# Kernel optimization log

Hardware: AMD Instinct MI355X
Metric: run time of the kernel (lower is better)

## Reference

```python
import jax, jax.numpy as jnp
import numpy as np

N = 50000
E = 800000
D = 64
H = 128


def setup_inputs() -> dict:
    key = jax.random.key(0)
    ks = jax.random.split(key, 8)
    x1 = jax.random.normal(ks[0], (N, D), dtype=jnp.float32)
    x2 = jax.random.normal(ks[1], (N, D), dtype=jnp.float32)
    edge_index1 = jax.random.randint(ks[2], (2, E), 0, N, dtype=jnp.int32)
    edge_index2 = jax.random.randint(ks[3], (2, E), 0, N, dtype=jnp.int32)
    W1 = jax.random.normal(ks[4], (2 * D, H), dtype=jnp.float32) * (1.0 / np.sqrt(2 * D))
    b1 = jnp.zeros((H,), dtype=jnp.float32)
    W2 = jax.random.normal(ks[5], (H, D), dtype=jnp.float32) * (1.0 / np.sqrt(H))
    b2 = jnp.zeros((D,), dtype=jnp.float32)
    return {"x1": x1, "x2": x2, "edge_index1": edge_index1, "edge_index2": edge_index2,
            "W1": W1, "b1": b1, "W2": W2, "b2": b2}


def _mlp(e, W1, b1, W2, b2):
    # edge MLP: Linear -> ReLU -> Linear
    h = jax.nn.relu(e @ W1 + b1)
    return h @ W2 + b2


def _scatter_max(vals, row, dim_size):
    # scatter-max aggregation; empty segments (which pyg scatter_ fills with 0)
    out = jax.ops.segment_max(vals, row, num_segments=dim_size)
    return jnp.where(jnp.isfinite(out), out, 0.0)


def reference(x1, x2, edge_index1, edge_index2, W1, b1, W2, b2):
    row1, col1 = edge_index1[0], edge_index1[1]
    # edge features from x1 -> x1: [E, 2D]
    e1 = jnp.concatenate([x1[row1], x1[col1] - x1[row1]], axis=1)
    out1 = _scatter_max(_mlp(e1, W1, b1, W2, b2), row1, x1.shape[0])

    row2, col2 = edge_index2[0], edge_index2[1]
    # edge features from x1 -> x2: [E, 2D]
    e2 = jnp.concatenate([x1[row2], x2[col2] - x1[row2]], axis=1)
    out2 = _scatter_max(_mlp(e2, W1, b1, W2, b2), row2, x2.shape[0])

    return jnp.concatenate([out1, out2], axis=-1)  # [N, 2*D]
```

## Files before the change

### kernel.cpp

```cpp
#include <hip/hip_runtime.h>

#define NN 50000
#define EE 800000
#define NTILES 12500
#define BPG 512
#define NPB 196

typedef _Float16 half8 __attribute__((ext_vector_type(8)));
typedef __attribute__((ext_vector_type(4))) float f32x4;
typedef __attribute__((ext_vector_type(4))) unsigned u32x4;

__device__ __forceinline__ unsigned enc(float f) {
    unsigned u = __float_as_uint(f);
    return u ^ (unsigned)(((int)u >> 31) | 0x80000000);
}
__device__ __forceinline__ float dec(unsigned u) {
    unsigned v = (u & 0x80000000u) ? (u & 0x7FFFFFFFu) : ~u;
    return __uint_as_float(v);
}

__global__ void decode_acc(unsigned* __restrict__ acc, int n) {
    int i = blockIdx.x * blockDim.x + threadIdx.x;
    if (i < n) {
        unsigned u = acc[i];
        ((float*)acc)[i] = (u == 0u) ? 0.0f : dec(u);
    }
}

__global__ __launch_bounds__(256)
void pre_k(const float* __restrict__ x1, const float* __restrict__ x2,
           const float* __restrict__ W1, const float* __restrict__ b1,
           _Float16* __restrict__ pre)
{
    const int j  = blockIdx.x / NPB;
    const int bb = blockIdx.x % NPB;
    const float* __restrict__ xs = (j == 2) ? x2 : x1;
    _Float16* __restrict__ out = pre + (size_t)j * NN * 128;

    const int lane = threadIdx.x & 63;
    const int w    = threadIdx.x >> 6;
    const int l15  = lane & 15;
    const int lg   = lane >> 4;
    const int rowbase = bb * 256 + w * 64;

    half8 af[4][2];
    #pragma unroll
    for (int m = 0; m < 4; ++m)
        #pragma unroll
        for (int ks = 0; ks < 2; ++ks) {
            int row = rowbase + 16 * m + l15;
            if (row > NN - 1) row = NN - 1;
            const float* p = xs + (size_t)row * 64 + 32 * ks + 8 * lg;
            half8 r;
            #pragma unroll
            for (int i = 0; i < 8; ++i) r[i] = (_Float16)p[i];
            af[m][ks] = r;
        }

    #pragma unroll 2
    for (int n = 0; n < 8; ++n) {
        half8 bf[2];
        #pragma unroll
        for (int ks = 0; ks < 2; ++ks) {
            half8 r;
            #pragma unroll
            for (int i = 0; i < 8; ++i) {
                int k = 32 * ks + 8 * lg + i;
                int o = 16 * n + l15;
                float wv = (j == 0)
                    ? (W1[(size_t)k * 128 + o] - W1[(size_t)(64 + k) * 128 + o])
                    :  W1[(size_t)(64 + k) * 128 + o];
                r[i] = (_Float16)wv;
            }
            bf[ks] = r;
        }
        float binit = (j == 0) ? b1[16 * n + l15] : 0.0f;
        f32x4 acc[4];
        #pragma unroll
        for (int m = 0; m < 4; ++m) {
            acc[m][0] = binit; acc[m][1] = binit;
            acc[m][2] = binit; acc[m][3] = binit;
        }
        #pragma unroll
        for (int ks = 0; ks < 2; ++ks)
            #pragma unroll
            for (int m = 0; m < 4; ++m)
                acc[m] = __builtin_amdgcn_mfma_f32_16x16x32_f16(
                    af[m][ks], bf[ks], acc[m], 0, 0, 0);
        #pragma unroll
        for (int m = 0; m < 4; ++m)
            #pragma unroll
            for (int r = 0; r < 4; ++r) {
                int row = rowbase + 16 * m + 4 * lg + r;
                if (row < NN)
                    out[(size_t)row * 128 + 16 * n + l15] = (_Float16)acc[m][r];
            }
    }
}

__global__ __launch_bounds__(256, 2)
void edge_mlp(const _Float16* __restrict__ pre,
              const int* __restrict__ ei1, const int* __restrict__ ei2,
              const float* __restrict__ W2, const float* __restrict__ b2,
              unsigned* __restrict__ acc)
{
    __shared__ short h_lds[2][64 * 128];
    __shared__ int srow[2][64];

    const int tid  = threadIdx.x;
    const int lane = tid & 63;
    const int l15  = lane & 15;
    const int lg   = lane >> 4;
    const int wid  = tid >> 6;
    const int w_h  = wid & 1;
    const int w_e  = wid >> 1;

    const int g     = (blockIdx.x >= BPG) ? 1 : 0;
    const int bslot = blockIdx.x & (BPG - 1);
    const int* __restrict__ ei = g ? ei2 : ei1;
    const _Float16* __restrict__ pa = pre;
    const _Float16* __restrict__ pb = pre + (size_t)(1 + g) * NN * 128;
    const int goff = g * 64;

    half8 b2f[4][2];
    #pragma unroll
    for (int s = 0; s < 4; ++s)
        #pragma unroll
        for (int n = 0; n < 2; ++n) {
            const float* p = W2 + (size_t)(32 * s + 8 * lg) * 64
                               + (w_h * 32 + 16 * n + l15);
            half8 r;
            #pragma unroll
            for (int i = 0; i < 8; ++i) r[i] = (_Float16)p[i * 64];
            b2f[s][n] = r;
        }
    float b2v[2];
    #pragma unroll
    for (int n = 0; n < 2; ++n) b2v[n] = b2[w_h * 32 + 16 * n + l15];

    const int ge = lane;
    const int gq = wid;
    const int swz = (ge & 15) << 3;

    int rcur, ccur, rnext, cnext;
    {
        int ta = bslot;
        rcur = ei[ta * 64 + ge];
        ccur = ei[EE + ta * 64 + ge];
        int tb = ta + BPG; if (tb >= NTILES) tb = NTILES - 1;
        rnext = ei[tb * 64 + ge];
        cnext = ei[EE + tb * 64 + ge];
    }
    uint4 ga0, ga1, ga2, ga3, gb0, gb1, gb2, gb3;
    {
        const uint4* ap = (const uint4*)(pa + (size_t)rcur * 128 + 32 * gq);
        const uint4* bp = (const uint4*)(pb + (size_t)ccur * 128 + 32 * gq);
        ga0 = ap[0]; ga1 = ap[1]; ga2 = ap[2]; ga3 = ap[3];
        gb0 = bp[0]; gb1 = bp[1]; gb2 = bp[2]; gb3 = bp[3];
    }

    const unsigned zu = 0u;
    int i = 0;
    for (int t = bslot; t < NTILES; t += BPG, ++i) {
        const int ib = i & 1;
        if (tid < 64) srow[ib][tid] = rcur;
        {
            short* hrow = &h_lds[ib][ge * 128];
            u32x4 h;
            #define COMBINE(A, B, K)                                           \
                {                                                              \
                    unsigned s0, s1, s2, s3;                                   \
                    asm("v_pk_add_f16 %0, %1, %2" : "=v"(s0) : "v"(A.x), "v"(B.x)); \
                    asm("v_pk_add_f16 %0, %1, %2" : "=v"(s1) : "v"(A.y), "v"(B.y)); \
                    asm("v_pk_add_f16 %0, %1, %2" : "=v"(s2) : "v"(A.z), "v"(B.z)); \
                    asm("v_pk_add_f16 %0, %1, %2" : "=v"(s3) : "v"(A.w), "v"(B.w)); \
                    asm("v_pk_max_f16 %0, %1, %2" : "=v"(s0) : "v"(s0), "v"(zu));   \
                    asm("v_pk_max_f16 %0, %1, %2" : "=v"(s1) : "v"(s1), "v"(zu));   \
                    asm("v_pk_max_f16 %0, %1, %2" : "=v"(s2) : "v"(s2), "v"(zu));   \
                    asm("v_pk_max_f16 %0, %1, %2" : "=v"(s3) : "v"(s3), "v"(zu));   \
                    h[0] = s0; h[1] = s1; h[2] = s2; h[3] = s3;                \
                    *(u32x4*)&hrow[(32 * gq + 8 * K) ^ swz] = h;               \
                }
            COMBINE(ga0, gb0, 0)
            COMBINE(ga1, gb1, 1)
            COMBINE(ga2, gb2, 2)
            COMBINE(ga3, gb3, 3)
            #undef COMBINE
        }

        rcur = rnext; ccur = cnext;
        {
            int t2 = t + 2 * BPG; if (t2 >= NTILES) t2 = NTILES - 1;
            rnext = ei[t2 * 64 + ge];
            cnext = ei[EE + t2 * 64 + ge];
        }
        if (t + BPG < NTILES) {
            const uint4* ap = (const uint4*)(pa + (size_t)rcur * 128 + 32 * gq);
            const uint4* bp = (const uint4*)(pb + (size_t)ccur * 128 + 32 * gq);
            ga0 = ap[0]; ga1 = ap[1]; ga2 = ap[2]; ga3 = ap[3];
            gb0 = bp[0]; gb1 = bp[1]; gb2 = bp[2]; gb3 = bp[3];
        }

        asm volatile("s_waitcnt lgkmcnt(0)\n\ts_barrier" ::: "memory");

        f32x4 acc2[2][2];
        #pragma unroll
        for (int m = 0; m < 2; ++m)
            #pragma unroll
            for (int n = 0; n < 2; ++n) {
                acc2[m][n][0] = b2v[n]; acc2[m][n][1] = b2v[n];
                acc2[m][n][2] = b2v[n]; acc2[m][n][3] = b2v[n];
            }
        __builtin_amdgcn_s_setprio(1);
        #pragma unroll
        for (int s = 0; s < 4; ++s) {
            half8 ha[2];
            #pragma unroll
            for (int m = 0; m < 2; ++m) {
                int e = w_e * 32 + 16 * m + l15;
                int sidx = e * 128 + ((32 * s + 8 * lg) ^ ((e & 15) << 3));
                ha[m] = *(const half8*)&h_lds[ib][sidx];
            }
            #pragma unroll
            for (int m = 0; m < 2; ++m)
                #pragma unroll
                for (int n = 0; n < 2; ++n)
                    acc2[m][n] = __builtin_amdgcn_mfma_f32_16x16x32_f16(
                        ha[m], b2f[s][n], acc2[m][n], 0, 0, 0);
        }
        __builtin_amdgcn_s_setprio(0);
        #pragma unroll
        for (int m = 0; m < 2; ++m) {
            int4 rows = *(const int4*)&srow[ib][w_e * 32 + 16 * m + 4 * lg];
            #pragma unroll
            for (int n = 0; n < 2; ++n) {
                int outc = w_h * 32 + 16 * n + l15;
                atomicMax(&acc[(size_t)rows.x * 128 + goff + outc], enc(acc2[m][n][0]));
                atomicMax(&acc[(size_t)rows.y * 128 + goff + outc], enc(acc2[m][n][1]));
                atomicMax(&acc[(size_t)rows.z * 128 + goff + outc], enc(acc2[m][n][2]));
                atomicMax(&acc[(size_t)rows.w * 128 + goff + outc], enc(acc2[m][n][3]));
            }
        }
    }
}

extern "C" void kernel_launch(void* const* d_in, const int* in_sizes, int n_in,
                              void* d_out, int out_size, void* d_ws, size_t ws_size,
                              hipStream_t stream) {
    const float* x1 = (const float*)d_in[0];
    const float* x2 = (const float*)d_in[1];
    const int*   ei1 = (const int*)d_in[2];
    const int*   ei2 = (const int*)d_in[3];
    const float* W1 = (const float*)d_in[4];
    const float* b1 = (const float*)d_in[5];
    const float* W2 = (const float*)d_in[6];
    const float* b2 = (const float*)d_in[7];
    unsigned* acc = (unsigned*)d_out;
    _Float16* pre = (_Float16*)d_ws;

    const int total = NN * 128;
    hipMemsetAsync(acc, 0, (size_t)total * sizeof(unsigned), stream);
    hipLaunchKernelGGL(pre_k, dim3(3 * NPB), dim3(256), 0, stream,
                       x1, x2, W1, b1, pre);
    hipLaunchKernelGGL(edge_mlp, dim3(2 * BPG), dim3(256), 0, stream,
                       pre, ei1, ei2, W2, b2, acc);
    hipLaunchKernelGGL(decode_acc, dim3((total + 255) / 256), dim3(256), 0, stream,
                       acc, total);
}
```

Measured before the change: 352.2 us.

## Sort edges by destination row and segment-reduce max before atomics

Adds a counting sort of edges by source row (histogram, block-partial sums, scan, scatter) so each edge_mlp block works through a contiguous range of sorted edges. Within 16-lane groups the MLP outputs are max-reduced across lanes that share a row, and only the segment tail issues the atomicMax calls, cutting atomic traffic. The MFMA operand order is swapped so each lane holds four consecutive output columns for one edge, BPG drops to 384 and the occupancy hint rises to 3 blocks. In exchange it adds five extra kernel launches plus a memset, and atomic histogram/scatter passes over 1.6M edges.

```diff
diff --git a/kernel.cpp b/kernel.cpp
--- a/kernel.cpp
+++ b/kernel.cpp
@@ -3,7 +3,8 @@
 #define NN 50000
 #define EE 800000
 #define NTILES 12500
-#define BPG 512
+#define BPG 384
+#define NB 98
 #define NPB 196
 
 typedef _Float16 half8 __attribute__((ext_vector_type(8)));
@@ -24,6 +25,87 @@
     if (i < n) {
         unsigned u = acc[i];
         ((float*)acc)[i] = (u == 0u) ? 0.0f : dec(u);
+    }
+}
+
+__global__ void hist_k(const int* __restrict__ ei1, const int* __restrict__ ei2,
+                       unsigned* __restrict__ cnt) {
+    int idx = blockIdx.x * blockDim.x + threadIdx.x;
+    if (idx < EE)           atomicAdd(&cnt[ei1[idx]], 1u);
+    else if (idx < 2 * EE)  atomicAdd(&cnt[NN + ei2[idx - EE]], 1u);
+}
+
+__global__ __launch_bounds__(512)
+void partial_k(const unsigned* __restrict__ cnt, unsigned* __restrict__ partial) {
+    int g = blockIdx.x / NB, b = blockIdx.x % NB;
+    int i = b * 512 + threadIdx.x;
+    unsigned x = (i < NN) ? cnt[g * NN + i] : 0u;
+    #pragma unroll
+    for (int o = 32; o; o >>= 1) x += __shfl_down(x, o, 64);
+    __shared__ unsigned ws[8];
+    int lane = threadIdx.x & 63, w = threadIdx.x >> 6;
+    if (lane == 0) ws[w] = x;
+    __syncthreads();
+    if (threadIdx.x == 0) {
+        unsigned s = 0;
+        #pragma unroll
+        for (int k = 0; k < 8; ++k) s += ws[k];
+        partial[g * NB + b] = s;
+    }
+}
+
+__global__ __launch_bounds__(128)
+void boff_k(const unsigned* __restrict__ partial, unsigned* __restrict__ boff) {
+    int g = threadIdx.x >> 6, lane = threadIdx.x & 63;
+    const unsigned* p = partial + g * NB;
+    unsigned* o = boff + g * NB;
+    unsigned x0 = p[lane];
+    unsigned v0 = x0;
+    #pragma unroll
+    for (int d = 1; d < 64; d <<= 1) { unsigned t = __shfl_up(v0, d, 64); if (lane >= d) v0 += t; }
+    unsigned sum0 = __shfl(v0, 63, 64);
+    unsigned x1 = (64 + lane < NB) ? p[64 + lane] : 0u;
+    unsigned v1 = x1;
+    #pragma unroll
+    for (int d = 1; d < 64; d <<= 1) { unsigned t = __shfl_up(v1, d, 64); if (lane >= d) v1 += t; }
+    o[lane] = v0 - x0;
+    if (64 + lane < NB) o[64 + lane] = sum0 + v1 - x1;
+}
+
+__global__ __launch_bounds__(512)
+void cur_k(const unsigned* __restrict__ cnt, const unsigned* __restrict__ boff,
+           unsigned* __restrict__ cur) {
+    int g = blockIdx.x / NB, b = blockIdx.x % NB;
+    int i = b * 512 + threadIdx.x;
+    unsigned x = (i < NN) ? cnt[g * NN + i] : 0u;
+    int lane = threadIdx.x & 63, w = threadIdx.x >> 6;
+    unsigned v = x;
+    #pragma unroll
+    for (int d = 1; d < 64; d <<= 1) { unsigned t = __shfl_up(v, d, 64); if (lane >= d) v += t; }
+    __shared__ unsigned ws[8], wso[8];
+    if (lane == 63) ws[w] = v;
+    __syncthreads();
+    if (threadIdx.x < 8) {
+        unsigned s = 0;
+        for (int k = 0; k < (int)threadIdx.x; ++k) s += ws[k];
+        wso[threadIdx.x] = s;
+    }
+    __syncthreads();
+    if (i < NN) cur[g * NN + i] = boff[g * NB + b] + wso[w] + v - x;
+}
+
+__global__ void scatter_k(const int* __restrict__ ei1, const int* __restrict__ ei2,
+                          unsigned* __restrict__ cur, uint2* __restrict__ se) {
+    int idx = blockIdx.x * blockDim.x + threadIdx.x;
+    if (idx < EE) {
+        int r = ei1[idx], c = ei1[EE + idx];
+        unsigned p = atomicAdd(&cur[r], 1u);
+        se[p] = make_uint2((unsigned)r, (unsigned)c);
+    } else if (idx < 2 * EE) {
+        int e = idx - EE;
+        int r = ei2[e], c = ei2[EE + e];
+        unsigned p = atomicAdd(&cur[NN + r], 1u);
+        se[EE + p] = make_uint2((unsigned)r, (unsigned)c);
     }
 }
 
@@ -98,9 +180,9 @@
     }
 }
 
-__global__ __launch_bounds__(256, 2)
+__global__ __launch_bounds__(256, 3)
 void edge_mlp(const _Float16* __restrict__ pre,
-              const int* __restrict__ ei1, const int* __restrict__ ei2,
+              const uint2* __restrict__ se,
               const float* __restrict__ W2, const float* __restrict__ b2,
               unsigned* __restrict__ acc)
 {
@@ -116,13 +198,16 @@
     const int w_e  = wid >> 1;
 
     const int g     = (blockIdx.x >= BPG) ? 1 : 0;
-    const int bslot = blockIdx.x & (BPG - 1);
-    const int* __restrict__ ei = g ? ei2 : ei1;
+    const int bslot = g ? (blockIdx.x - BPG) : blockIdx.x;
+    const uint2* __restrict__ sed = se + (size_t)g * EE;
     const _Float16* __restrict__ pa = pre;
     const _Float16* __restrict__ pb = pre + (size_t)(1 + g) * NN * 128;
     const int goff = g * 64;
 
-    half8 b2f[4][2];
+    const int t0 = (bslot * NTILES) / BPG;
+    const int t1 = ((bslot + 1) * NTILES) / BPG;
+
+    half8 w2f[4][2];
     #pragma unroll
     for (int s = 0; s < 4; ++s)
         #pragma unroll
@@ -132,11 +217,12 @@
             half8 r;
             #pragma unroll
             for (int i = 0; i < 8; ++i) r[i] = (_Float16)p[i * 64];
-            b2f[s][n] = r;
-        }
-    float b2v[2];
-    #pragma unroll
-    for (int n = 0; n < 2; ++n) b2v[n] = b2[w_h * 32 + 16 * n + l15];
+            w2f[s][n] = r;
+        }
+    float4 b2v4[2];
+    #pragma unroll
+    for (int n = 0; n < 2; ++n)
+        b2v4[n] = *(const float4*)(b2 + w_h * 32 + 16 * n + 4 * lg);
 
     const int ge = lane;
     const int gq = wid;
@@ -144,12 +230,11 @@
 
     int rcur, ccur, rnext, cnext;
     {
-        int ta = bslot;
-        rcur = ei[ta * 64 + ge];
-        ccur = ei[EE + ta * 64 + ge];
-        int tb = ta + BPG; if (tb >= NTILES) tb = NTILES - 1;
-        rnext = ei[tb * 64 + ge];
-        cnext = ei[EE + tb * 64 + ge];
+        uint2 a = sed[t0 * 64 + ge];
+        rcur = (int)a.x; ccur = (int)a.y;
+        int tb = min(t0 + 1, t1 - 1);
+        uint2 b = sed[tb * 64 + ge];
+        rnext = (int)b.x; cnext = (int)b.y;
     }
     uint4 ga0, ga1, ga2, ga3, gb0, gb1, gb2, gb3;
     {
@@ -161,7 +246,7 @@
 
     const unsigned zu = 0u;
     int i = 0;
-    for (int t = bslot; t < NTILES; t += BPG, ++i) {
+    for (int t = t0; t < t1; ++t, ++i) {
         const int ib = i & 1;
         if (tid < 64) srow[ib][tid] = rcur;
         {
@@ -190,11 +275,11 @@
 
         rcur = rnext; ccur = cnext;
         {
-            int t2 = t + 2 * BPG; if (t2 >= NTILES) t2 = NTILES - 1;
-            rnext = ei[t2 * 64 + ge];
-            cnext = ei[EE + t2 * 64 + ge];
-        }
-        if (t + BPG < NTILES) {
+            int t2 = min(t + 2, t1 - 1);
+            uint2 b = sed[t2 * 64 + ge];
+            rnext = (int)b.x; cnext = (int)b.y;
+        }
+        if (t + 1 < t1) {
             const uint4* ap = (const uint4*)(pa + (size_t)rcur * 128 + 32 * gq);
             const uint4* bp = (const uint4*)(pb + (size_t)ccur * 128 + 32 * gq);
             ga0 = ap[0]; ga1 = ap[1]; ga2 = ap[2]; ga3 = ap[3];
@@ -208,37 +293,58 @@
         for (int m = 0; m < 2; ++m)
             #pragma unroll
             for (int n = 0; n < 2; ++n) {
-                acc2[m][n][0] = b2v[n]; acc2[m][n][1] = b2v[n];
-                acc2[m][n][2] = b2v[n]; acc2[m][n][3] = b2v[n];
+                acc2[m][n][0] = b2v4[n].x; acc2[m][n][1] = b2v4[n].y;
+                acc2[m][n][2] = b2v4[n].z; acc2[m][n][3] = b2v4[n].w;
             }
         __builtin_amdgcn_s_setprio(1);
         #pragma unroll
         for (int s = 0; s < 4; ++s) {
-            half8 ha[2];
+            half8 hb[2];
             #pragma unroll
             for (int m = 0; m < 2; ++m) {
                 int e = w_e * 32 + 16 * m + l15;
                 int sidx = e * 128 + ((32 * s + 8 * lg) ^ ((e & 15) << 3));
-                ha[m] = *(const half8*)&h_lds[ib][sidx];
+                hb[m] = *(const half8*)&h_lds[ib][sidx];
             }
             #pragma unroll
             for (int m = 0; m < 2; ++m)
                 #pragma unroll
                 for (int n = 0; n < 2; ++n)
                     acc2[m][n] = __builtin_amdgcn_mfma_f32_16x16x32_f16(
-                        ha[m], b2f[s][n], acc2[m][n], 0, 0, 0);
+                        w2f[s][n], hb[m], acc2[m][n], 0, 0, 0);
         }
         __builtin_amdgcn_s_setprio(0);
+
         #pragma unroll
         for (int m = 0; m < 2; ++m) {
-            int4 rows = *(const int4*)&srow[ib][w_e * 32 + 16 * m + 4 * lg];
-            #pragma unroll
-            for (int n = 0; n < 2; ++n) {
-                int outc = w_h * 32 + 16 * n + l15;
-                atomicMax(&acc[(size_t)rows.x * 128 + goff + outc], enc(acc2[m][n][0]));
-                atomicMax(&acc[(size_t)rows.y * 128 + goff + outc], enc(acc2[m][n][1]));
-                atomicMax(&acc[(size_t)rows.z * 128 + goff + outc], enc(acc2[m][n][2]));
-                atomicMax(&acc[(size_t)rows.w * 128 + goff + outc], enc(acc2[m][n][3]));
+            int myrow = srow[ib][w_e * 32 + 16 * m + l15];
+            f32x4 v0 = acc2[m][0], v1 = acc2[m][1];
+            #pragma unroll
+            for (int d = 1; d < 16; d <<= 1) {
+                int pr = __shfl_up(myrow, d, 16);
+                float a0 = __shfl_up(v0[0], d, 16), a1 = __shfl_up(v0[1], d, 16);
+                float a2 = __shfl_up(v0[2], d, 16), a3 = __shfl_up(v0[3], d, 16);
+                float c0 = __shfl_up(v1[0], d, 16), c1 = __shfl_up(v1[1], d, 16);
+                float c2 = __shfl_up(v1[2], d, 16), c3 = __shfl_up(v1[3], d, 16);
+                if (l15 >= d && pr == myrow) {
+                    v0[0] = fmaxf(v0[0], a0); v0[1] = fmaxf(v0[1], a1);
+                    v0[2] = fmaxf(v0[2], a2); v0[3] = fmaxf(v0[3], a3);
+                    v1[0] = fmaxf(v1[0], c0); v1[1] = fmaxf(v1[1], c1);
+                    v1[2] = fmaxf(v1[2], c2); v1[3] = fmaxf(v1[3], c3);
+                }
+            }
+            int nr = __shfl_down(myrow, 1, 16);
+            bool tail = (l15 == 15) || (nr != myrow);
+            if (tail) {
+                unsigned* dst = acc + (size_t)myrow * 128 + goff + w_h * 32 + 4 * lg;
+                atomicMax(dst + 0,      enc(v0[0]));
+                atomicMax(dst + 1,      enc(v0[1]));
+                atomicMax(dst + 2,      enc(v0[2]));
+                atomicMax(dst + 3,      enc(v0[3]));
+                atomicMax(dst + 16 + 0, enc(v1[0]));
+                atomicMax(dst + 16 + 1, enc(v1[1]));
+                atomicMax(dst + 16 + 2, enc(v1[2]));
+                atomicMax(dst + 16 + 3, enc(v1[3]));
             }
         }
     }
@@ -256,14 +362,30 @@
     const float* W2 = (const float*)d_in[6];
     const float* b2 = (const float*)d_in[7];
     unsigned* acc = (unsigned*)d_out;
-    _Float16* pre = (_Float16*)d_ws;
+
+    unsigned* w = (unsigned*)d_ws;
+    unsigned* cnt     = w;
+    unsigned* partial = w + 100000;
+    unsigned* boff    = w + 100200;
+    unsigned* cur     = w + 100400;
+    uint2*    se      = (uint2*)(w + 200400);
+    _Float16* pre     = (_Float16*)(w + 3400400);
 
     const int total = NN * 128;
+    hipMemsetAsync(cnt, 0, 2 * NN * sizeof(unsigned), stream);
     hipMemsetAsync(acc, 0, (size_t)total * sizeof(unsigned), stream);
+
+    hipLaunchKernelGGL(hist_k, dim3((2 * EE + 255) / 256), dim3(256), 0, stream,
+                       ei1, ei2, cnt);
+    hipLaunchKernelGGL(partial_k, dim3(2 * NB), dim3(512), 0, stream, cnt, partial);
+    hipLaunchKernelGGL(boff_k, dim3(1), dim3(128), 0, stream, partial, boff);
+    hipLaunchKernelGGL(cur_k, dim3(2 * NB), dim3(512), 0, stream, cnt, boff, cur);
+    hipLaunchKernelGGL(scatter_k, dim3((2 * EE + 255) / 256), dim3(256), 0, stream,
+                       ei1, ei2, cur, se);
     hipLaunchKernelGGL(pre_k, dim3(3 * NPB), dim3(256), 0, stream,
                        x1, x2, W1, b1, pre);
     hipLaunchKernelGGL(edge_mlp, dim3(2 * BPG), dim3(256), 0, stream,
-                       pre, ei1, ei2, W2, b2, acc);
+                       pre, se, W2, b2, acc);
     hipLaunchKernelGGL(decode_acc, dim3((total + 255) / 256), dim3(256), 0, stream,
                        acc, total);
 }
```

Result: slower. 461.5 us (+31.0%).
